# Kernel tuning notes

Measured on AMD Instinct MI355X. Metric: run time of the kernel, lower is better.

The kernel has to match this reference:

```python
import jax, jax.numpy as jnp
import numpy as np

N = 1_000_000
D = 256
NUM_SEGMENTS = 4096  # = batch.max() + 1


def setup_inputs() -> dict:
    key = jax.random.key(0)
    ks = jax.random.split(key, 8)
    x = jax.random.normal(ks[0], (N, D), dtype=jnp.float32)
    batch = jnp.sort(jax.random.randint(ks[1], (N,), 0, NUM_SEGMENTS, dtype=jnp.int32))
    s = 1.0 / np.sqrt(D)
    s2 = 1.0 / np.sqrt(2 * D)
    W_in = jax.random.uniform(ks[2], (D, D), jnp.float32, -s, s)
    b_in = jax.random.uniform(ks[3], (D,), jnp.float32, -s, s)
    W1 = jax.random.uniform(ks[4], (D, 2 * D), jnp.float32, -s, s)
    b1 = jax.random.uniform(ks[5], (2 * D,), jnp.float32, -s, s)
    W2 = jax.random.uniform(ks[6], (2 * D, D), jnp.float32, -s2, s2)
    b2 = jax.random.uniform(ks[7], (D,), jnp.float32, -s2, s2)
    return {"x": x, "batch": batch, "W_in": W_in, "b_in": b_in,
            "W1": W1, "b1": b1, "W2": W2, "b2": b2}


def reference(x, batch, W_in, b_in, W1, b1, W2, b2):
    # proj_in: Linear(d, d)
    h = x @ W_in + b_in                                   # [N, D]
    # scatter_add segment-sum over batch ids -> [num_graphs, D]
    pooled = jax.ops.segment_sum(h, batch, num_segments=NUM_SEGMENTS)
    # proj_out: Linear(d, 2d) -> ReLU -> Linear(2d, d)
    out = jax.nn.relu(pooled @ W1 + b1) @ W2 + b2         # [num_graphs, D]
    return out
```

## Files before the change

### kernel.cpp

```cpp
#include <hip/hip_runtime.h>

#define DDIM 256
#define HDIM 512

typedef float f32x4 __attribute__((ext_vector_type(4)));
typedef short bf16x8 __attribute__((ext_vector_type(8)));

__device__ inline unsigned short f2bf(float f) {
  unsigned int u = __float_as_uint(f);
  u += 0x7fff + ((u >> 16) & 1);
  return (unsigned short)(u >> 16);
}

__global__ __launch_bounds__(256) void fused_main_kernel(
    const float* __restrict__ x, const int* __restrict__ batch,
    const float* __restrict__ W_in, const float* __restrict__ b_in,
    const float* __restrict__ W1, const float* __restrict__ W2,
    unsigned short* __restrict__ WfT, unsigned short* __restrict__ W2T,
    float* __restrict__ bvec, unsigned short* __restrict__ Sb,
    float* __restrict__ counts, int N, int G) {
  const int b = blockIdx.x;

  if (b < 2 * DDIM + 2) {
    __shared__ float vrow[DDIM];
    const bool is_b = (b >= 2 * DDIM);
    const int i = is_b ? 0 : (b >> 1);
    const int half = is_b ? (b - 2 * DDIM) : (b & 1);
    const float* src = is_b ? b_in : (W_in + (size_t)i * DDIM);
    vrow[threadIdx.x] = src[threadIdx.x];
    __syncthreads();

    const int j = half * 256 + threadIdx.x;
    float h = 0.f;
#pragma unroll 8
    for (int k = 0; k < DDIM; ++k) h += vrow[k] * W1[(size_t)k * HDIM + j];
    if (is_b) bvec[j] = h;
    else WfT[(size_t)j * DDIM + i] = f2bf(h);
    return;
  }
  if (b < 2 * DDIM + 2 + DDIM) {
    const int n = b - (2 * DDIM + 2);
    for (int k = threadIdx.x; k < HDIM; k += 256)
      W2T[(size_t)n * HDIM + k] = f2bf(W2[(size_t)k * DDIM + n]);
    return;
  }

  const int g = b - (2 * DDIM + 2 + DDIM);
  __shared__ int se[2];
  __shared__ float red[3][DDIM];

  if (threadIdx.x < 2) {
    const int target = g + threadIdx.x;
    int lo = 0, hi = N;
    while (lo < hi) {
      const int mid = (lo + hi) >> 1;
      if (batch[mid] < target) lo = mid + 1;
      else hi = mid;
    }
    se[threadIdx.x] = lo;
  }
  __syncthreads();
  const int start = se[0], end = se[1];

  const int w  = threadIdx.x >> 6;
  const int c4 = (threadIdx.x & 63) << 2;
  const float* xp = x + c4;

  f32x4 a0 = {0.f, 0.f, 0.f, 0.f};
  f32x4 a1 = {0.f, 0.f, 0.f, 0.f};
  f32x4 a2 = {0.f, 0.f, 0.f, 0.f};
  f32x4 a3 = {0.f, 0.f, 0.f, 0.f};

  int i = start + w;
  for (; i + 12 < end; i += 16) {
    const f32x4 v0 = __builtin_nontemporal_load(
        reinterpret_cast<const f32x4*>(xp + (size_t)i * DDIM));
    const f32x4 v1 = __builtin_nontemporal_load(
        reinterpret_cast<const f32x4*>(xp + (size_t)(i + 4) * DDIM));
    const f32x4 v2 = __builtin_nontemporal_load(
        reinterpret_cast<const f32x4*>(xp + (size_t)(i + 8) * DDIM));
    const f32x4 v3 = __builtin_nontemporal_load(
        reinterpret_cast<const f32x4*>(xp + (size_t)(i + 12) * DDIM));
    a0 += v0;
    a1 += v1;
    a2 += v2;
    a3 += v3;
  }
  for (; i < end; i += 4) {
    const f32x4 v0 = __builtin_nontemporal_load(
        reinterpret_cast<const f32x4*>(xp + (size_t)i * DDIM));
    a0 += v0;
  }
  a0 += a1;
  a2 += a3;
  a0 += a2;

  if (w != 0) *reinterpret_cast<f32x4*>(&red[w - 1][c4]) = a0;
  __syncthreads();
  if (w == 0) {
#pragma unroll
    for (int r = 0; r < 3; ++r) {
      a0 += *reinterpret_cast<const f32x4*>(&red[r][c4]);
    }
    ushort4 sv;
    sv.x = f2bf(a0.x);
    sv.y = f2bf(a0.y);
    sv.z = f2bf(a0.z);
    sv.w = f2bf(a0.w);
    *reinterpret_cast<ushort4*>(Sb + (size_t)g * DDIM + c4) = sv;
    if (threadIdx.x == 0) counts[g] = (float)(end - start);
  }
}

template <int K, bool RELU, int BIAS_MODE, bool OUTBF>
__global__ __launch_bounds__(256) void mfma_gemm_kernel(
    int N, const unsigned short* __restrict__ A,
    const unsigned short* __restrict__ BT, const float* __restrict__ bias,
    const float* __restrict__ bvec, const float* __restrict__ counts,
    float* __restrict__ Cf, unsigned short* __restrict__ Cb) {
  const int m0 = blockIdx.y * 64, n0 = blockIdx.x * 64;
  const int tid = threadIdx.x;
  const int wid = tid >> 6, lane = tid & 63;
  const int wr = wid >> 1, wc = wid & 1;
  const int l15 = lane & 15, lk8 = (lane >> 4) << 3;

  const unsigned short* Ap0 = A + (size_t)(m0 + wr * 32 + l15) * K + lk8;
  const unsigned short* Ap1 = Ap0 + (size_t)16 * K;
  const unsigned short* Bp0 = BT + (size_t)(n0 + wc * 32 + l15) * K + lk8;
  const unsigned short* Bp1 = Bp0 + (size_t)16 * K;

  f32x4 acc00 = {0.f, 0.f, 0.f, 0.f};
  f32x4 acc01 = {0.f, 0.f, 0.f, 0.f};
  f32x4 acc10 = {0.f, 0.f, 0.f, 0.f};
  f32x4 acc11 = {0.f, 0.f, 0.f, 0.f};

#pragma unroll
  for (int k0 = 0; k0 < K; k0 += 32) {
    const bf16x8 a0 = *reinterpret_cast<const bf16x8*>(Ap0 + k0);
    const bf16x8 a1 = *reinterpret_cast<const bf16x8*>(Ap1 + k0);
    const bf16x8 b0 = *reinterpret_cast<const bf16x8*>(Bp0 + k0);
    const bf16x8 b1 = *reinterpret_cast<const bf16x8*>(Bp1 + k0);
    acc00 = __builtin_amdgcn_mfma_f32_16x16x32_bf16(a0, b0, acc00, 0, 0, 0);
    acc01 = __builtin_amdgcn_mfma_f32_16x16x32_bf16(a0, b1, acc01, 0, 0, 0);
    acc10 = __builtin_amdgcn_mfma_f32_16x16x32_bf16(a1, b0, acc10, 0, 0, 0);
    acc11 = __builtin_amdgcn_mfma_f32_16x16x32_bf16(a1, b1, acc11, 0, 0, 0);
  }

  const int rbase = m0 + wr * 32 + ((lane >> 4) << 2);
  const int cbase = n0 + wc * 32 + l15;
#pragma unroll
  for (int si = 0; si < 2; ++si) {
#pragma unroll
    for (int sj = 0; sj < 2; ++sj) {
      const f32x4 ac = (si == 0) ? (sj == 0 ? acc00 : acc01)
                                 : (sj == 0 ? acc10 : acc11);
      const int col = cbase + sj * 16;
      const float bj = (BIAS_MODE >= 1) ? bias[col] : 0.f;
      const float vj = (BIAS_MODE == 2) ? bvec[col] : 0.f;
#pragma unroll
      for (int r = 0; r < 4; ++r) {
        const int row = rbase + si * 16 + r;
        float v = ac[r] + bj;
        if (BIAS_MODE == 2) v += counts[row] * vj;
        if (RELU) v = fmaxf(v, 0.f);
        if (OUTBF) Cb[(size_t)row * N + col] = f2bf(v);
        else       Cf[(size_t)row * N + col] = v;
      }
    }
  }
}

extern "C" void kernel_launch(void* const* d_in, const int* in_sizes, int n_in,
                              void* d_out, int out_size, void* d_ws,
                              size_t ws_size, hipStream_t stream) {
  const float* x     = (const float*)d_in[0];
  const int*   batch = (const int*)d_in[1];
  const float* W_in  = (const float*)d_in[2];
  const float* b_in  = (const float*)d_in[3];
  const float* W1    = (const float*)d_in[4];
  const float* b1    = (const float*)d_in[5];
  const float* W2    = (const float*)d_in[6];
  const float* b2    = (const float*)d_in[7];
  float* out = (float*)d_out;

  const int N = in_sizes[1];
  const int G = out_size / DDIM;

  char* wsb = (char*)d_ws;
  size_t off = 0;
  unsigned short* WfT = (unsigned short*)(wsb + off);  off += (size_t)HDIM * DDIM * 2;
  unsigned short* W2T = (unsigned short*)(wsb + off);  off += (size_t)DDIM * HDIM * 2;
  float* bvec   = (float*)(wsb + off);                 off += (size_t)HDIM * 4;
  float* counts = (float*)(wsb + off);                 off += (size_t)G * 4;
  unsigned short* Sb = (unsigned short*)(wsb + off);   off += (size_t)G * DDIM * 2;
  unsigned short* Hb = (unsigned short*)(wsb + off);

  fused_main_kernel<<<2 * DDIM + 2 + DDIM + G, 256, 0, stream>>>(
      x, batch, W_in, b_in, W1, W2, WfT, W2T, bvec, Sb, counts, N, G);

  mfma_gemm_kernel<DDIM, true, 2, true>
      <<<dim3(HDIM / 64, G / 64), 256, 0, stream>>>(
          HDIM, Sb, WfT, b1, bvec, counts, nullptr, Hb);

  mfma_gemm_kernel<HDIM, false, 1, false>
      <<<dim3(DDIM / 64, G / 64), 256, 0, stream>>>(
          DDIM, Hb, W2T, b2, nullptr, nullptr, out, nullptr);
}
```

Before: 190.0 us.

## Fuse the two MLP GEMMs into one kernel with the hidden layer kept in LDS

```diff
diff --git a/kernel.cpp b/kernel.cpp
--- a/kernel.cpp
+++ b/kernel.cpp
@@ -112,60 +112,72 @@
   }
 }
 
-template <int K, bool RELU, int BIAS_MODE, bool OUTBF>
-__global__ __launch_bounds__(256) void mfma_gemm_kernel(
-    int N, const unsigned short* __restrict__ A,
-    const unsigned short* __restrict__ BT, const float* __restrict__ bias,
-    const float* __restrict__ bvec, const float* __restrict__ counts,
-    float* __restrict__ Cf, unsigned short* __restrict__ Cb) {
-  const int m0 = blockIdx.y * 64, n0 = blockIdx.x * 64;
+__global__ __launch_bounds__(256) void mlp_kernel(
+    const unsigned short* __restrict__ Sb,
+    const unsigned short* __restrict__ WfT,
+    const unsigned short* __restrict__ W2T, const float* __restrict__ bvec,
+    const float* __restrict__ b1, const float* __restrict__ b2,
+    const float* __restrict__ counts, float* __restrict__ out) {
+  __shared__ unsigned short Hs[16 * HDIM];
   const int tid = threadIdx.x;
   const int wid = tid >> 6, lane = tid & 63;
-  const int wr = wid >> 1, wc = wid & 1;
   const int l15 = lane & 15, lk8 = (lane >> 4) << 3;
-
-  const unsigned short* Ap0 = A + (size_t)(m0 + wr * 32 + l15) * K + lk8;
-  const unsigned short* Ap1 = Ap0 + (size_t)16 * K;
-  const unsigned short* Bp0 = BT + (size_t)(n0 + wc * 32 + l15) * K + lk8;
-  const unsigned short* Bp1 = Bp0 + (size_t)16 * K;
-
-  f32x4 acc00 = {0.f, 0.f, 0.f, 0.f};
-  f32x4 acc01 = {0.f, 0.f, 0.f, 0.f};
-  f32x4 acc10 = {0.f, 0.f, 0.f, 0.f};
-  f32x4 acc11 = {0.f, 0.f, 0.f, 0.f};
-
-#pragma unroll
-  for (int k0 = 0; k0 < K; k0 += 32) {
-    const bf16x8 a0 = *reinterpret_cast<const bf16x8*>(Ap0 + k0);
-    const bf16x8 a1 = *reinterpret_cast<const bf16x8*>(Ap1 + k0);
-    const bf16x8 b0 = *reinterpret_cast<const bf16x8*>(Bp0 + k0);
-    const bf16x8 b1 = *reinterpret_cast<const bf16x8*>(Bp1 + k0);
-    acc00 = __builtin_amdgcn_mfma_f32_16x16x32_bf16(a0, b0, acc00, 0, 0, 0);
-    acc01 = __builtin_amdgcn_mfma_f32_16x16x32_bf16(a0, b1, acc01, 0, 0, 0);
-    acc10 = __builtin_amdgcn_mfma_f32_16x16x32_bf16(a1, b0, acc10, 0, 0, 0);
-    acc11 = __builtin_amdgcn_mfma_f32_16x16x32_bf16(a1, b1, acc11, 0, 0, 0);
-  }
-
-  const int rbase = m0 + wr * 32 + ((lane >> 4) << 2);
-  const int cbase = n0 + wc * 32 + l15;
-#pragma unroll
-  for (int si = 0; si < 2; ++si) {
-#pragma unroll
-    for (int sj = 0; sj < 2; ++sj) {
-      const f32x4 ac = (si == 0) ? (sj == 0 ? acc00 : acc01)
-                                 : (sj == 0 ? acc10 : acc11);
-      const int col = cbase + sj * 16;
-      const float bj = (BIAS_MODE >= 1) ? bias[col] : 0.f;
-      const float vj = (BIAS_MODE == 2) ? bvec[col] : 0.f;
-#pragma unroll
-      for (int r = 0; r < 4; ++r) {
-        const int row = rbase + si * 16 + r;
-        float v = ac[r] + bj;
-        if (BIAS_MODE == 2) v += counts[row] * vj;
-        if (RELU) v = fmaxf(v, 0.f);
-        if (OUTBF) Cb[(size_t)row * N + col] = f2bf(v);
-        else       Cf[(size_t)row * N + col] = v;
-      }
+  const int rbase = (lane >> 4) << 2;
+  const int m0 = blockIdx.x * 16;
+
+  const unsigned short* Ap = Sb + (size_t)(m0 + l15) * DDIM + lk8;
+  const unsigned short* Bp = WfT + (size_t)(wid * 128 + l15) * DDIM + lk8;
+
+  f32x4 acc[8] = {};
+#pragma unroll
+  for (int k0 = 0; k0 < DDIM; k0 += 32) {
+    const bf16x8 a = *reinterpret_cast<const bf16x8*>(Ap + k0);
+#pragma unroll
+    for (int sj = 0; sj < 8; ++sj) {
+      const bf16x8 bb =
+          *reinterpret_cast<const bf16x8*>(Bp + (size_t)sj * 16 * DDIM + k0);
+      acc[sj] = __builtin_amdgcn_mfma_f32_16x16x32_bf16(a, bb, acc[sj], 0, 0, 0);
+    }
+  }
+  char* hsb = (char*)Hs;
+#pragma unroll
+  for (int sj = 0; sj < 8; ++sj) {
+    const int col = wid * 128 + sj * 16 + l15;
+    const float vj = bvec[col];
+    const float bj = b1[col];
+#pragma unroll
+    for (int r = 0; r < 4; ++r) {
+      const int row = rbase + r;
+      float v = acc[sj][r] + counts[m0 + row] * vj + bj;
+      v = fmaxf(v, 0.f);
+      const int byte = (row << 10) + (col << 1);
+      *(unsigned short*)(hsb + (byte ^ ((row & 7) << 4))) = f2bf(v);
+    }
+  }
+  __syncthreads();
+
+  const unsigned short* B2p = W2T + (size_t)(wid * 64 + l15) * HDIM + lk8;
+  f32x4 acc2[4] = {};
+#pragma unroll
+  for (int k0 = 0; k0 < HDIM; k0 += 32) {
+    const int kb = (l15 << 10) + ((lk8 + k0) << 1);
+    const bf16x8 a =
+        *reinterpret_cast<const bf16x8*>(hsb + (kb ^ ((l15 & 7) << 4)));
+#pragma unroll
+    for (int sj = 0; sj < 4; ++sj) {
+      const bf16x8 bb =
+          *reinterpret_cast<const bf16x8*>(B2p + (size_t)sj * 16 * HDIM + k0);
+      acc2[sj] = __builtin_amdgcn_mfma_f32_16x16x32_bf16(a, bb, acc2[sj], 0, 0, 0);
+    }
+  }
+#pragma unroll
+  for (int sj = 0; sj < 4; ++sj) {
+    const int col = wid * 64 + sj * 16 + l15;
+    const float bj = b2[col];
+#pragma unroll
+    for (int r = 0; r < 4; ++r) {
+      const int row = m0 + rbase + r;
+      out[(size_t)row * DDIM + col] = acc2[sj][r] + bj;
     }
   }
 }
@@ -192,17 +204,11 @@
   unsigned short* W2T = (unsigned short*)(wsb + off);  off += (size_t)DDIM * HDIM * 2;
   float* bvec   = (float*)(wsb + off);                 off += (size_t)HDIM * 4;
   float* counts = (float*)(wsb + off);                 off += (size_t)G * 4;
-  unsigned short* Sb = (unsigned short*)(wsb + off);   off += (size_t)G * DDIM * 2;
-  unsigned short* Hb = (unsigned short*)(wsb + off);
+  unsigned short* Sb = (unsigned short*)(wsb + off);
 
   fused_main_kernel<<<2 * DDIM + 2 + DDIM + G, 256, 0, stream>>>(
       x, batch, W_in, b_in, W1, W2, WfT, W2T, bvec, Sb, counts, N, G);
 
-  mfma_gemm_kernel<DDIM, true, 2, true>
-      <<<dim3(HDIM / 64, G / 64), 256, 0, stream>>>(
-          HDIM, Sb, WfT, b1, bvec, counts, nullptr, Hb);
-
-  mfma_gemm_kernel<HDIM, false, 1, false>
-      <<<dim3(DDIM / 64, G / 64), 256, 0, stream>>>(
-          DDIM, Hb, W2T, b2, nullptr, nullptr, out, nullptr);
-}
+  mlp_kernel<<<G / 16, 256, 0, stream>>>(Sb, WfT, W2T, bvec, b1, b2, counts,
+                                         out);
+}
```

After: 186.0 us, median of 2. 2.1% less time.
